# Performance work log

Hardware: AMD Instinct MI355X
Metric: run time of the kernel (lower is better)

Reference implementation:

```python
import jax, jax.numpy as jnp
import numpy as np

K = 20
EPS = 1e-5


def _bn(h, g, b, axes):
    m = jnp.mean(h, axes, keepdims=True)
    v = jnp.var(h, axes, keepdims=True)
    return (h - m) * jax.lax.rsqrt(v + EPS) * g + b


def _edge_feat(h):
    # h: [B,N,D] -> edge features [B,N,K,2D] = concat(central, neighbor-central)
    sq = jnp.sum(h * h, -1)
    # negative squared pairwise distance (larger = closer)
    adj = 2.0 * jnp.einsum('bnd,bmd->bnm', h, h) - sq[:, :, None] - sq[:, None, :]
    idx = jax.lax.top_k(adj, K)[1]  # [B,N,K] nearest (incl. self)
    nbr = jax.vmap(lambda hb, ib: hb[ib])(h, idx)  # [B,N,K,D]
    ctr = jnp.broadcast_to(h[:, :, None, :], nbr.shape)
    return jnp.concatenate([ctr, nbr - ctr], -1)


def _edge_layer(h, W, b, g, be):
    # 1x1 conv over edge features, relu THEN batchnorm (matches torch: bn(relu(conv))), max over K
    ef = _edge_feat(h)
    z = jax.nn.relu(jnp.einsum('bnkc,oc->bnko', ef, W) + b)
    z = _bn(z, g, be, (0, 1, 2))
    return jnp.max(z, axis=2)  # [B,N,O]


def _c1d(h, W, b):
    return jnp.einsum('bcl,oc->bol', h, W) + b[None, :, None]


def _bnc(h, g, b):
    m = jnp.mean(h, (0, 2), keepdims=True)
    v = jnp.var(h, (0, 2), keepdims=True)
    return (h - m) * jax.lax.rsqrt(v + EPS) * g[None, :, None] + b[None, :, None]


def _forward(x, rand_grid, W1, b1, g1, be1, W2, b2, g2, be2, W3, b3, g3, be3,
             W4, b4, g4, be4, W5, b5, g5, be5, lW, lb, lg, lbe,
             dW1, db1, dg1, dbe1, dW2, db2, dg2, dbe2, dW3, db3, dg3, dbe3, dW4, db4):
    pts = jnp.transpose(x, (0, 2, 1))  # [B,N,3]
    x1 = _edge_layer(pts, W1, b1, g1, be1)   # [B,N,64]
    x2 = _edge_layer(x1, W2, b2, g2, be2)    # [B,N,64]
    x3 = _edge_layer(x2, W3, b3, g3, be3)    # [B,N,64]
    x4 = _edge_layer(x3, W4, b4, g4, be4)    # [B,N,128]
    cat = jnp.concatenate([x1, x2, x3, x4], -1)  # [B,N,320]
    z = jax.nn.relu(jnp.einsum('bnc,oc->bno', cat, W5) + b5)
    z = _bn(z, g5, be5, (0, 1))
    glob = jnp.max(z, axis=1)  # [B,1024]
    lat = glob @ lW.T + lb
    lat = jax.nn.relu(_bn(lat, lg, lbe, (0,)))  # [B,1024]
    B, C = lat.shape
    P = rand_grid.shape[2]
    y = jnp.concatenate([rand_grid, jnp.broadcast_to(lat[:, :, None], (B, C, P))], axis=1)  # [B,1026,P]
    h = jax.nn.relu(_bnc(_c1d(y, dW1, db1), dg1, dbe1))
    h = jax.nn.relu(_bnc(_c1d(h, dW2, db2), dg2, dbe2))
    h = jax.nn.relu(_bnc(_c1d(h, dW3, db3), dg3, dbe3))
    return jnp.tanh(_c1d(h, dW4, db4))  # [B,3,P]


def setup_inputs() -> dict:
    key = jax.random.key(0)
    ks = iter(jax.random.split(key, 64))
    B, N, BOT = 8, 2048, 1024
    D = BOT + 2  # 1026
    f32 = jnp.float32

    def w(o, c):
        return jax.random.normal(next(ks), (o, c), dtype=f32) * 0.05

    def bnp(c):
        return jnp.ones((c,), f32), jnp.zeros((c,), f32)

    inp = {
        'x': jax.random.normal(next(ks), (B, 3, N), dtype=f32),
        'rand_grid': jax.random.uniform(next(ks), (B, 2, N), dtype=f32),
    }
    enc = [(64, 6), (64, 128), (64, 128), (128, 128), (1024, 320)]
    for i, (o, c) in enumerate(enc, 1):
        inp[f'W{i}'] = w(o, c)
        inp[f'b{i}'] = jnp.zeros((o,), f32)
        inp[f'g{i}'], inp[f'be{i}'] = bnp(o)
    inp['lW'] = w(BOT, 1024)
    inp['lb'] = jnp.zeros((BOT,), f32)
    inp['lg'], inp['lbe'] = bnp(BOT)
    dec = [(D, D), (D // 2, D), (D // 4, D // 2), (3, D // 4)]
    for i, (o, c) in enumerate(dec, 1):
        inp[f'dW{i}'] = w(o, c)
        inp[f'db{i}'] = jnp.zeros((o,), f32)
        if i < 4:
            inp[f'dg{i}'], inp[f'dbe{i}'] = bnp(o)
    return inp


def reference(x, rand_grid, W1, b1, g1, be1, W2, b2, g2, be2, W3, b3, g3, be3,
              W4, b4, g4, be4, W5, b5, g5, be5, lW, lb, lg, lbe,
              dW1, db1, dg1, dbe1, dW2, db2, dg2, dbe2, dW3, db3, dg3, dbe3, dW4, db4):
    return _forward(x, rand_grid, W1, b1, g1, be1, W2, b2, g2, be2, W3, b3, g3, be3,
                    W4, b4, g4, be4, W5, b5, g5, be5, lW, lb, lg, lbe,
                    dW1, db1, dg1, dbe1, dW2, db2, dg2, dbe2, dW3, db3, dg3, dbe3, dW4, db4)
```

## Files before the change

kernel.cpp:

```cpp
#include <hip/hip_runtime.h>
#include <math.h>

constexpr int NB = 8;
constexpr int NN = 2048;
constexpr int NK = 20;
constexpr int NP = 2048;


__global__ void transpose_x_kernel(const float* __restrict__ x, float* __restrict__ pts) {
  int gid = blockIdx.x * 256 + threadIdx.x;
  if (gid >= NB * NN * 3) return;
  int c = gid % 3;
  int n = (gid / 3) % NN;
  int b = gid / (3 * NN);
  pts[gid] = x[(b * 3 + c) * NN + n];
}

__global__ void transpose_mat_ld(const float* __restrict__ src, float* __restrict__ dst, int R,
                                 int C, int ldd) {
  __shared__ float tile[32][33];
  int c0 = blockIdx.x * 32, r0 = blockIdx.y * 32;
  int tx = threadIdx.x & 31, ty = threadIdx.x >> 5;
  for (int i = ty; i < 32; i += 8) {
    int r = r0 + i, c = c0 + tx;
    tile[i][tx] = (r < R && c < C) ? src[(size_t)r * C + c] : 0.f;
  }
  __syncthreads();
  for (int i = ty; i < 32; i += 8) {
    int c = c0 + i, r = r0 + tx;
    if (r < R && c < C) dst[(size_t)c * ldd + r] = tile[tx][i];
  }
}

__global__ void knn3_fused_kernel(const float* __restrict__ pts, int* __restrict__ idx) {
  __shared__ float sm[3][NN];
  int t = threadIdx.x;
  int l = t & 63, w = t >> 6;
  int gb = blockIdx.x;
  int b = gb >> 9;
  int n0 = (gb & 511) * 4;
  const float* base = pts + (size_t)b * NN * 3;
  for (int e = t; e < NN * 3; e += 256) {
    int col = e / 3, d = e - col * 3;
    sm[d][col] = base[e];
  }
  __syncthreads();
  int n = n0 + w;
  float c0 = sm[0][n], c1 = sm[1][n], c2 = sm[2][n];
  float v[32];
#pragma unroll
  for (int j = 0; j < 32; j++) {
    int col = j * 64 + l;
    float d0 = c0 - sm[0][col];
    float d1 = c1 - sm[1][col];
    float d2 = c2 - sm[2][col];
    float acc = 0.f;
    acc = fmaf(d0, d0, acc);
    acc = fmaf(d1, d1, acc);
    acc = fmaf(d2, d2, acc);
    v[j] = -acc;
  }
  int mykm = 0;
  for (int k = 0; k < NK; k++) {
    float bv = v[0];
    int bj = 0;
#pragma unroll
    for (int j = 1; j < 32; j++) {
      if (v[j] > bv) { bv = v[j]; bj = j; }
    }
    int gm = bj * 64 + l;
#pragma unroll
    for (int off = 32; off; off >>= 1) {
      float ov = __shfl_xor(bv, off, 64);
      int om = __shfl_xor(gm, off, 64);
      if (ov > bv || (ov == bv && om < gm)) { bv = ov; gm = om; }
    }
    if (l == k) mykm = gm;
    int jb = gm >> 6, lb = gm & 63;
#pragma unroll
    for (int j = 0; j < 32; j++)
      if (j == jb && l == lb) v[j] = -3e38f;
  }
  if (l < NK) idx[((size_t)(b * NN + n)) * NK + l] = mykm;
}

__global__ __launch_bounds__(256, 2) void knn64_fused4_kernel(const float* __restrict__ h, int ld,
                                                              int coff, int* __restrict__ idx) {
  __shared__ float sft[64][128];
  __shared__ float sctr[16][64];
  int t = threadIdx.x;
  int l = t & 63, w = t >> 6;
  int n0 = blockIdx.x * 16;
  int b = blockIdx.y;
  const float* rows = h + (size_t)b * NN * ld + coff;
  for (int e = t; e < 16 * 64; e += 256) {
    int r = e >> 6, d = e & 63;
    sctr[r][d] = rows[(size_t)(n0 + r) * ld + d];
  }
  int colg = t & 127;
  int dh = (t >> 7) * 32;
  float v[4][32];
#pragma unroll
  for (int ct = 0; ct < 16; ct++) {
    __syncthreads();
    {
      const float* src = &rows[(size_t)(ct * 128 + colg) * ld + dh];
#pragma unroll
      for (int q = 0; q < 8; q++) {
        float4 f = *(const float4*)(src + q * 4);
        sft[dh + q * 4 + 0][colg] = f.x;
        sft[dh + q * 4 + 1][colg] = f.y;
        sft[dh + q * 4 + 2][colg] = f.z;
        sft[dh + q * 4 + 3][colg] = f.w;
      }
    }
    __syncthreads();
    float a00 = 0.f, a01 = 0.f, a10 = 0.f, a11 = 0.f;
    float a20 = 0.f, a21 = 0.f, a30 = 0.f, a31 = 0.f;
#pragma unroll 8
    for (int d = 0; d < 64; d++) {
      float f0 = sft[d][l];
      float f1 = sft[d][64 + l];
      float c0v = sctr[4 * w + 0][d];
      float c1v = sctr[4 * w + 1][d];
      float c2v = sctr[4 * w + 2][d];
      float c3v = sctr[4 * w + 3][d];
      float e;
      e = c0v - f0; a00 = fmaf(e, e, a00);
      e = c0v - f1; a01 = fmaf(e, e, a01);
      e = c1v - f0; a10 = fmaf(e, e, a10);
      e = c1v - f1; a11 = fmaf(e, e, a11);
      e = c2v - f0; a20 = fmaf(e, e, a20);
      e = c2v - f1; a21 = fmaf(e, e, a21);
      e = c3v - f0; a30 = fmaf(e, e, a30);
      e = c3v - f1; a31 = fmaf(e, e, a31);
    }
    v[0][2 * ct] = -a00; v[0][2 * ct + 1] = -a01;
    v[1][2 * ct] = -a10; v[1][2 * ct + 1] = -a11;
    v[2][2 * ct] = -a20; v[2][2 * ct + 1] = -a21;
    v[3][2 * ct] = -a30; v[3][2 * ct + 1] = -a31;
  }
#pragma unroll
  for (int ci = 0; ci < 4; ci++) {
    int mykm = 0;
    for (int k = 0; k < NK; k++) {
      float bv = v[ci][0];
      int bj = 0;
#pragma unroll
      for (int j = 1; j < 32; j++) {
        if (v[ci][j] > bv) { bv = v[ci][j]; bj = j; }
      }
      int gm = ((bj >> 1) << 7) + ((bj & 1) << 6) + l;
#pragma unroll
      for (int off = 32; off; off >>= 1) {
        float ov = __shfl_xor(bv, off, 64);
        int om = __shfl_xor(gm, off, 64);
        if (ov > bv || (ov == bv && om < gm)) { bv = ov; gm = om; }
      }
      if (l == k) mykm = gm;
      int jb = ((gm >> 7) << 1) + ((gm >> 6) & 1);
      int lb = gm & 63;
#pragma unroll
      for (int j = 0; j < 32; j++)
        if (j == jb && l == lb) v[ci][j] = -3e38f;
    }
    if (l < NK) idx[((size_t)(b * NN + n0 + 4 * w + ci)) * NK + l] = mykm;
  }
}

__global__ void weff_kernel(const float* __restrict__ W, int O, int D, float* __restrict__ Weff) {
  int i = blockIdx.x * 256 + threadIdx.x;
  if (i >= 2 * O * D) return;
  int o = i / D, d = i - o * D;
  float v;
  if (o < O) v = W[(size_t)o * 2 * D + d] - W[(size_t)o * 2 * D + D + d];
  else v = W[(size_t)(o - O) * 2 * D + D + d];
  Weff[i] = v;
}

template <int M2, int D>
__global__ __launch_bounds__(256, 4) void pgemm_kernel(const float* __restrict__ h, int ld,
                                                       int coff, const float* __restrict__ Weff,
                                                       const float* __restrict__ bias,
                                                       float* __restrict__ P) {
  constexpr int O = M2 / 2;
  constexpr int GRP = 256 / M2;
  constexpr int NR = 8 / GRP;
  __shared__ float sh[8][D == 3 ? 4 : 68];
  int t = threadIdx.x;
  int n0 = blockIdx.x * 8;
  const float* base = h + coff;
  if constexpr (D == 64) {
    if (t < 128) {
      int r = t >> 4, q = (t & 15) * 4;
      *(float4*)&sh[r][q] = *(const float4*)&base[(size_t)(n0 + r) * ld + q];
    }
  } else {
    if (t < 24) {
      int r = t / 3, c = t - r * 3;
      sh[r][c] = base[(size_t)(n0 + r) * ld + c];
    }
  }
  __syncthreads();
  int o = t % M2;
  int gi = t / M2;
  float acc[NR];
  float bz = (o < O) ? bias[o] : 0.f;
#pragma unroll
  for (int j = 0; j < NR; j++) acc[j] = bz;
  const float* wr = Weff + (size_t)o * D;
  if constexpr (D == 64) {
#pragma unroll
    for (int d4 = 0; d4 < 16; d4++) {
      float4 w4 = *(const float4*)&wr[d4 * 4];
#pragma unroll
      for (int j = 0; j < NR; j++) {
        float4 e4 = *(const float4*)&sh[gi * NR + j][d4 * 4];
        acc[j] = fmaf(w4.x, e4.x, acc[j]);
        acc[j] = fmaf(w4.y, e4.y, acc[j]);
        acc[j] = fmaf(w4.z, e4.z, acc[j]);
        acc[j] = fmaf(w4.w, e4.w, acc[j]);
      }
    }
  } else {
    float w0 = wr[0], w1 = wr[1], w2 = wr[2];
#pragma unroll
    for (int j = 0; j < NR; j++) {
      int r = gi * NR + j;
      acc[j] = fmaf(w0, sh[r][0], fmaf(w1, sh[r][1], fmaf(w2, sh[r][2], acc[j])));
    }
  }
#pragma unroll
  for (int j = 0; j < NR; j++)
    P[(size_t)(n0 + gi * NR + j) * M2 + o] = acc[j];
}

template <int O>
__global__ __launch_bounds__(256, 8) void combine_kernel(const float* __restrict__ P,
                                                         const int* __restrict__ idx,
                                                         float* __restrict__ zmax,
                                                         float* __restrict__ zmin,
                                                         float* __restrict__ psum,
                                                         float* __restrict__ psq) {
  constexpr int CPB = 256 / O;
  constexpr int M2 = 2 * O;
  __shared__ int sidx[CPB * NK];
  int t = threadIdx.x;
  int bn0 = blockIdx.x * CPB;
  if (t < CPB * NK) sidx[t] = idx[(size_t)bn0 * NK + t];
  __syncthreads();
  int g = t / O, o = t % O;
  int bn = bn0 + g;
  int b = bn >> 11;
  float p1 = P[(size_t)bn * M2 + o];
  const float* P2 = P + (size_t)b * NN * M2 + O + o;
  float s = 0.f, sq = 0.f, mx = -3e38f, mn = 3e38f;
#pragma unroll
  for (int k = 0; k < NK; k++) {
    int nb = sidx[g * NK + k];
    float z = fmaxf(p1 + P2[(size_t)nb * M2], 0.f);
    s += z;
    sq = fmaf(z, z, sq);
    mx = fmaxf(mx, z);
    mn = fminf(mn, z);
  }
  zmax[(size_t)bn * O + o] = mx;
  zmin[(size_t)bn * O + o] = mn;
  psum[(size_t)o * (NB * NN) + bn] = s;
  psq[(size_t)o * (NB * NN) + bn] = sq;
}

__global__ void edge_reduce_kernel(const float* __restrict__ psum, const float* __restrict__ psq,
                                   const float* __restrict__ g, const float* __restrict__ be,
                                   float* __restrict__ scale, float* __restrict__ shift,
                                   double inv_n) {
  int o = blockIdx.x, t = threadIdx.x;
  double s = 0.0, q = 0.0;
  const float* ps = psum + (size_t)o * (NB * NN);
  const float* pq = psq + (size_t)o * (NB * NN);
  for (int i = t; i < NB * NN; i += 256) { s += (double)ps[i]; q += (double)pq[i]; }
  __shared__ double rs[256], rq[256];
  rs[t] = s; rq[t] = q;
  __syncthreads();
  for (int st = 128; st; st >>= 1) {
    if (t < st) { rs[t] += rs[t + st]; rq[t] += rq[t + st]; }
    __syncthreads();
  }
  if (t == 0) {
    double mean = rs[0] * inv_n;
    double var = rq[0] * inv_n - mean * mean;
    double r = 1.0 / sqrt(var + 1e-5);
    double sc = (double)g[o] * r;
    scale[o] = (float)sc;
    shift[o] = (float)((double)be[o] - mean * sc);
  }
}

__global__ void edge_affine_kernel(const float* __restrict__ zmax, const float* __restrict__ zmin,
                                   const float* __restrict__ scale, const float* __restrict__ shift,
                                   float* __restrict__ cat, int O, int coff_out) {
  int gid = blockIdx.x * 256 + threadIdx.x;
  int o = gid % O;
  int bn = gid / O;
  float sc = scale[o];
  float v = (sc >= 0.f) ? zmax[gid] : zmin[gid];
  cat[(size_t)bn * 320 + coff_out + o] = fmaf(sc, v, shift[o]);
}

__global__ __launch_bounds__(256, 2) void gemm5_64_kernel(const float* __restrict__ cat,
                                                          const float* __restrict__ W5t,
                                                          const float* __restrict__ b5,
                                                          float* __restrict__ z5) {
  __shared__ float sA[32][64];
  __shared__ float sB[32][128];
  int t = threadIdx.x;
  int r0 = blockIdx.x * 64, m0 = blockIdx.y * 128;
  int arow = t & 63, ach = (t >> 6) * 8;
  int blr = t >> 4, blc = (t & 15) * 8;
  int tx = t & 15, ty = t >> 4;
  float acc[4][8] = {};
  float rA[8], rB[16];

  auto gload = [&](int c0) {
    const float* pa = &cat[(size_t)(r0 + arow) * 320 + c0 + ach];
    float4 a0 = *(const float4*)pa;
    float4 a1 = *(const float4*)(pa + 4);
    rA[0] = a0.x; rA[1] = a0.y; rA[2] = a0.z; rA[3] = a0.w;
    rA[4] = a1.x; rA[5] = a1.y; rA[6] = a1.z; rA[7] = a1.w;
    const float* pb = &W5t[(size_t)(c0 + blr) * 1024 + m0 + blc];
    float4 b0 = *(const float4*)pb;
    float4 b1 = *(const float4*)(pb + 4);
    rB[0] = b0.x; rB[1] = b0.y; rB[2] = b0.z; rB[3] = b0.w;
    rB[4] = b1.x; rB[5] = b1.y; rB[6] = b1.z; rB[7] = b1.w;
    const float* pb2 = &W5t[(size_t)(c0 + 16 + blr) * 1024 + m0 + blc];
    float4 c4 = *(const float4*)pb2;
    float4 c5 = *(const float4*)(pb2 + 4);
    rB[8] = c4.x; rB[9] = c4.y; rB[10] = c4.z; rB[11] = c4.w;
    rB[12] = c5.x; rB[13] = c5.y; rB[14] = c5.z; rB[15] = c5.w;
  };
  auto ldswrite = [&]() {
#pragma unroll
    for (int j = 0; j < 8; j++) sA[ach + j][arow] = rA[j];
    float4 w0, w1;
    w0.x = rB[0]; w0.y = rB[1]; w0.z = rB[2]; w0.w = rB[3];
    w1.x = rB[4]; w1.y = rB[5]; w1.z = rB[6]; w1.w = rB[7];
    *(float4*)&sB[blr][blc] = w0;
    *(float4*)&sB[blr][blc + 4] = w1;
    w0.x = rB[8]; w0.y = rB[9]; w0.z = rB[10]; w0.w = rB[11];
    w1.x = rB[12]; w1.y = rB[13]; w1.z = rB[14]; w1.w = rB[15];
    *(float4*)&sB[16 + blr][blc] = w0;
    *(float4*)&sB[16 + blr][blc + 4] = w1;
  };

  gload(0);
  for (int kt = 0; kt < 10; kt++) {
    __syncthreads();
    ldswrite();
    __syncthreads();
    if (kt + 1 < 10) gload((kt + 1) * 32);
#pragma unroll
    for (int c = 0; c < 32; c++) {
      float4 a0 = *(const float4*)&sA[c][ty * 4];
      float4 b0 = *(const float4*)&sB[c][tx * 4];
      float4 b1 = *(const float4*)&sB[c][64 + tx * 4];
      float av[4] = {a0.x, a0.y, a0.z, a0.w};
      float bv[8] = {b0.x, b0.y, b0.z, b0.w, b1.x, b1.y, b1.z, b1.w};
#pragma unroll
      for (int i = 0; i < 4; i++)
#pragma unroll
        for (int j = 0; j < 8; j++) acc[i][j] = fmaf(av[i], bv[j], acc[i][j]);
    }
  }
  float bj[8];
#pragma unroll
  for (int j = 0; j < 8; j++)
    bj[j] = b5[m0 + (j < 4 ? tx * 4 + j : 64 + tx * 4 + (j - 4))];
#pragma unroll
  for (int i = 0; i < 4; i++) {
    int r = r0 + ty * 4 + i;
    float* dst = &z5[(size_t)r * 1024 + m0];
    float4 q0, q1;
    q0.x = fmaxf(acc[i][0] + bj[0], 0.f);
    q0.y = fmaxf(acc[i][1] + bj[1], 0.f);
    q0.z = fmaxf(acc[i][2] + bj[2], 0.f);
    q0.w = fmaxf(acc[i][3] + bj[3], 0.f);
    q1.x = fmaxf(acc[i][4] + bj[4], 0.f);
    q1.y = fmaxf(acc[i][5] + bj[5], 0.f);
    q1.z = fmaxf(acc[i][6] + bj[6], 0.f);
    q1.w = fmaxf(acc[i][7] + bj[7], 0.f);
    *(float4*)&dst[tx * 4] = q0;
    *(float4*)&dst[64 + tx * 4] = q1;
  }
}

__global__ void stats5_kernel(const float* __restrict__ z5, double* __restrict__ psum5,
                              double* __restrict__ psq5, float* __restrict__ pmax5,
                              float* __restrict__ pmin5) {
  int j = blockIdx.x, t = threadIdx.x;
  int row0 = j * 64;
  double s0 = 0, s1 = 0, s2 = 0, s3 = 0, q0 = 0, q1 = 0, q2 = 0, q3 = 0;
  float4 mx = {-3e38f, -3e38f, -3e38f, -3e38f}, mn = {3e38f, 3e38f, 3e38f, 3e38f};
  for (int r = 0; r < 64; r++) {
    float4 v = *(const float4*)&z5[(size_t)(row0 + r) * 1024 + t * 4];
    s0 += v.x; s1 += v.y; s2 += v.z; s3 += v.w;
    q0 += (double)v.x * v.x; q1 += (double)v.y * v.y;
    q2 += (double)v.z * v.z; q3 += (double)v.w * v.w;
    mx.x = fmaxf(mx.x, v.x); mx.y = fmaxf(mx.y, v.y); mx.z = fmaxf(mx.z, v.z); mx.w = fmaxf(mx.w, v.w);
    mn.x = fminf(mn.x, v.x); mn.y = fminf(mn.y, v.y); mn.z = fminf(mn.z, v.z); mn.w = fminf(mn.w, v.w);
  }
  size_t base = (size_t)j * 1024 + t * 4;
  psum5[base + 0] = s0; psum5[base + 1] = s1; psum5[base + 2] = s2; psum5[base + 3] = s3;
  psq5[base + 0] = q0; psq5[base + 1] = q1; psq5[base + 2] = q2; psq5[base + 3] = q3;
  *(float4*)&pmax5[base] = mx;
  *(float4*)&pmin5[base] = mn;
}

__global__ void reduce5_glob_kernel(const double* __restrict__ psum5, const double* __restrict__ psq5,
                                    const float* __restrict__ pmax5, const float* __restrict__ pmin5,
                                    const float* __restrict__ g5, const float* __restrict__ be5,
                                    float* __restrict__ glob) {
  int o = blockIdx.x * 256 + threadIdx.x;
  double s = 0.0, q = 0.0;
  for (int j = 0; j < 256; j++) {
    s += psum5[(size_t)j * 1024 + o];
    q += psq5[(size_t)j * 1024 + o];
  }
  double mean = s * (1.0 / 16384.0);
  double var = q * (1.0 / 16384.0) - mean * mean;
  double r = 1.0 / sqrt(var + 1e-5);
  double scd = (double)g5[o] * r;
  float sc = (float)scd;
  float sh = (float)((double)be5[o] - mean * scd);
  for (int b = 0; b < 8; b++) {
    float m;
    if (sc >= 0.f) {
      m = -3e38f;
      for (int jj = 0; jj < 32; jj++) m = fmaxf(m, pmax5[(size_t)(b * 32 + jj) * 1024 + o]);
    } else {
      m = 3e38f;
      for (int jj = 0; jj < 32; jj++) m = fminf(m, pmin5[(size_t)(b * 32 + jj) * 1024 + o]);
    }
    glob[b * 1024 + o] = fmaf(sc, m, sh);
  }
}

__global__ void fc_kernel(const float* __restrict__ in, const float* __restrict__ Wt, int ld,
                          int coff, const float* __restrict__ bias, float* __restrict__ out,
                          int Ci, int Co) {
  __shared__ float sin_[1024];
  __shared__ float red[8][32];
  int b = blockIdx.x, t = threadIdx.x;
  for (int e = t; e < Ci; e += 256) sin_[e] = in[(size_t)b * Ci + e];
  __syncthreads();
  int o = blockIdx.y * 32 + (t & 31);
  int cg = t >> 5;
  int cn = Ci / 8;
  float p = 0.f;
  if (o < Co) {
    for (int c = cg * cn; c < (cg + 1) * cn; c++)
      p = fmaf(Wt[(size_t)(c + coff) * ld + o], sin_[c], p);
  }
  red[cg][t & 31] = p;
  __syncthreads();
  if (cg == 0 && o < Co) {
    float s = red[0][t] + red[1][t] + red[2][t] + red[3][t] + red[4][t] + red[5][t] + red[6][t] +
              red[7][t];
    out[(size_t)b * Co + o] = s + bias[o];
  }
}

__global__ void lat_bn_kernel(const float* __restrict__ latp, const float* __restrict__ lg,
                              const float* __restrict__ lbe, float* __restrict__ lat) {
  int o = blockIdx.x * 256 + threadIdx.x;
  float v[8];
  double s = 0.0, q = 0.0;
  for (int b = 0; b < 8; b++) {
    v[b] = latp[b * 1024 + o];
    s += (double)v[b];
    q += (double)v[b] * (double)v[b];
  }
  double mean = s * 0.125;
  double var = q * 0.125 - mean * mean;
  double r = 1.0 / sqrt(var + 1e-5);
  double gd = (double)lg[o], bd = (double)lbe[o];
  for (int b = 0; b < 8; b++) {
    float z = (float)(((double)v[b] - mean) * r * gd + bd);
    lat[b * 1024 + o] = fmaxf(z, 0.f);
  }
}

__global__ void dec1_z_kernel(const float* __restrict__ rg, const float* __restrict__ dW1t,
                              const float* __restrict__ u, float* __restrict__ z1) {
  int bo = blockIdx.x;
  int b = bo / 1026;
  int o = bo - b * 1026;
  int t = threadIdx.x;
  float w0 = dW1t[o], w1 = dW1t[1026 + o], ub = u[bo];
  const float4* r0 = (const float4*)(rg + (size_t)b * 2 * NP);
  const float4* r1 = (const float4*)(rg + (size_t)b * 2 * NP + NP);
  float4* zr = (float4*)(z1 + (size_t)bo * NP);
  for (int i = t; i < NP / 4; i += 256) {
    float4 a = r0[i], c = r1[i], rr;
    rr.x = fmaf(w0, a.x, fmaf(w1, c.x, ub));
    rr.y = fmaf(w0, a.y, fmaf(w1, c.y, ub));
    rr.z = fmaf(w0, a.z, fmaf(w1, c.z, ub));
    rr.w = fmaf(w0, a.w, fmaf(w1, c.w, ub));
    zr[i] = rr;
  }
}

__global__ void dstats_kernel(const float* __restrict__ z, int C, const float* __restrict__ g,
                              const float* __restrict__ be, float* __restrict__ scale,
                              float* __restrict__ shift) {
  int o = blockIdx.x, t = threadIdx.x;
  double s = 0.0, q = 0.0;
  for (int b = 0; b < 8; b++) {
    const float4* row = (const float4*)(z + ((size_t)b * C + o) * NP);
    for (int i = t; i < NP / 4; i += 256) {
      float4 v = row[i];
      s += (double)v.x + (double)v.y + (double)v.z + (double)v.w;
      q += (double)v.x * v.x + (double)v.y * v.y + (double)v.z * v.z + (double)v.w * v.w;
    }
  }
  __shared__ double rs[256], rq[256];
  rs[t] = s; rq[t] = q;
  __syncthreads();
  for (int st = 128; st; st >>= 1) {
    if (t < st) { rs[t] += rs[t + st]; rq[t] += rq[t + st]; }
    __syncthreads();
  }
  if (t == 0) {
    double inv = 1.0 / (8.0 * NP);
    double mean = rs[0] * inv;
    double var = rq[0] * inv - mean * mean;
    double r = 1.0 / sqrt(var + 1e-5);
    double sc = (double)g[o] * r;
    scale[o] = (float)sc;
    shift[o] = (float)((double)be[o] - mean * sc);
  }
}

template <int NMT>
__global__ __launch_bounds__(256, 2) void dec_gemm64s_kernel(
    const float* __restrict__ zin, const float* __restrict__ Wt, int ldA,
    const float* __restrict__ bias, const float* __restrict__ scale,
    const float* __restrict__ shift, float* __restrict__ zout, int Ci, int Co) {
  __shared__ float sA[32][64];
  __shared__ float sB[32][128];
  int bid = blockIdx.x;
  int gl = bid & 7;
  int q = bid >> 3;
  int gh = q / NMT;
  int mt = q - gh * NMT;
  int g = gl + (gh << 3);
  int pt = g & 15;
  int b = g >> 4;
  int m0 = mt * 64, p0 = pt * 128;
  int t = threadIdx.x;
  int lr = t >> 4, lcA = (t & 15) * 4, lcB = (t & 15) * 8;
  int tx = t & 15, ty = t >> 4;
  int numK = (Ci + 31) >> 5;
  float acc[4][8] = {};
  float rA[8], rB[16];

  auto gloadhalf = [&](int c, float* ra, float* rb) {
#pragma unroll
    for (int j = 0; j < 4; j++) ra[j] = 0.f;
#pragma unroll
    for (int j = 0; j < 8; j++) rb[j] = 0.f;
    if (c < Ci) {
      int mb = m0 + lcA;
      if (mb + 4 <= Co) {
        float4 a0 = *(const float4*)&Wt[(size_t)c * ldA + mb];
        ra[0] = a0.x; ra[1] = a0.y; ra[2] = a0.z; ra[3] = a0.w;
      } else {
#pragma unroll
        for (int j = 0; j < 4; j++)
          if (mb + j < Co) ra[j] = Wt[(size_t)c * ldA + mb + j];
      }
      float sc = scale[c], sh = shift[c];
      const float* src = &zin[((size_t)b * Ci + c) * NP + p0 + lcB];
      float4 z0 = *(const float4*)src;
      float4 z1 = *(const float4*)(src + 4);
      rb[0] = fmaxf(fmaf(sc, z0.x, sh), 0.f);
      rb[1] = fmaxf(fmaf(sc, z0.y, sh), 0.f);
      rb[2] = fmaxf(fmaf(sc, z0.z, sh), 0.f);
      rb[3] = fmaxf(fmaf(sc, z0.w, sh), 0.f);
      rb[4] = fmaxf(fmaf(sc, z1.x, sh), 0.f);
      rb[5] = fmaxf(fmaf(sc, z1.y, sh), 0.f);
      rb[6] = fmaxf(fmaf(sc, z1.z, sh), 0.f);
      rb[7] = fmaxf(fmaf(sc, z1.w, sh), 0.f);
    }
  };
  auto gload = [&](int kt) {
    gloadhalf(kt * 32 + lr, rA, rB);
    gloadhalf(kt * 32 + 16 + lr, rA + 4, rB + 8);
  };
  auto ldswrite = [&]() {
    float4 v0;
    v0.x = rA[0]; v0.y = rA[1]; v0.z = rA[2]; v0.w = rA[3];
    *(float4*)&sA[lr][lcA] = v0;
    v0.x = rA[4]; v0.y = rA[5]; v0.z = rA[6]; v0.w = rA[7];
    *(float4*)&sA[16 + lr][lcA] = v0;
    float4 w0, w1;
    w0.x = rB[0]; w0.y = rB[1]; w0.z = rB[2]; w0.w = rB[3];
    w1.x = rB[4]; w1.y = rB[5]; w1.z = rB[6]; w1.w = rB[7];
    *(float4*)&sB[lr][lcB] = w0;
    *(float4*)&sB[lr][lcB + 4] = w1;
    w0.x = rB[8]; w0.y = rB[9]; w0.z = rB[10]; w0.w = rB[11];
    w1.x = rB[12]; w1.y = rB[13]; w1.z = rB[14]; w1.w = rB[15];
    *(float4*)&sB[16 + lr][lcB] = w0;
    *(float4*)&sB[16 + lr][lcB + 4] = w1;
  };

  gload(0);
  for (int kt = 0; kt < numK; kt++) {
    __syncthreads();
    ldswrite();
    __syncthreads();
    if (kt + 1 < numK) gload(kt + 1);
#pragma unroll
    for (int c = 0; c < 32; c++) {
      float4 a0 = *(const float4*)&sA[c][ty * 4];
      float4 b0 = *(const float4*)&sB[c][tx * 4];
      float4 b1 = *(const float4*)&sB[c][64 + tx * 4];
      float av[4] = {a0.x, a0.y, a0.z, a0.w};
      float bv[8] = {b0.x, b0.y, b0.z, b0.w, b1.x, b1.y, b1.z, b1.w};
#pragma unroll
      for (int i = 0; i < 4; i++)
#pragma unroll
        for (int j = 0; j < 8; j++) acc[i][j] = fmaf(av[i], bv[j], acc[i][j]);
    }
  }
#pragma unroll
  for (int i = 0; i < 4; i++) {
    int m = m0 + ty * 4 + i;
    if (m < Co) {
      float bv = bias[m];
      float* dst = &zout[((size_t)b * Co + m) * NP + p0];
      float4 q0, q1;
      q0.x = acc[i][0] + bv; q0.y = acc[i][1] + bv;
      q0.z = acc[i][2] + bv; q0.w = acc[i][3] + bv;
      q1.x = acc[i][4] + bv; q1.y = acc[i][5] + bv;
      q1.z = acc[i][6] + bv; q1.w = acc[i][7] + bv;
      *(float4*)&dst[tx * 4] = q0;
      *(float4*)&dst[64 + tx * 4] = q1;
    }
  }
}

__global__ void dec_final_kernel(const float* __restrict__ z3, const float* __restrict__ dW4,
                                 const float* __restrict__ db4, const float* __restrict__ scale,
                                 const float* __restrict__ shift, float* __restrict__ out) {
  __shared__ float w4[3 * 256];
  __shared__ float sc[256], sh[256];
  __shared__ float red[4][64][3];
  int b = blockIdx.x, pc = blockIdx.y, t = threadIdx.x;
  for (int e = t; e < 768; e += 256) w4[e] = dW4[e];
  sc[t] = scale[t];
  sh[t] = shift[t];
  __syncthreads();
  int tp = t & 63, tc = t >> 6;
  int p = pc * 64 + tp;
  float a0 = 0.f, a1 = 0.f, a2 = 0.f;
  for (int c = tc * 64; c < tc * 64 + 64; c++) {
    float hv = fmaxf(fmaf(sc[c], z3[((size_t)(b * 256 + c)) * NP + p], sh[c]), 0.f);
    a0 = fmaf(w4[c], hv, a0);
    a1 = fmaf(w4[256 + c], hv, a1);
    a2 = fmaf(w4[512 + c], hv, a2);
  }
  red[tc][tp][0] = a0;
  red[tc][tp][1] = a1;
  red[tc][tp][2] = a2;
  __syncthreads();
  if (tc == 0) {
    a0 = red[0][tp][0] + red[1][tp][0] + red[2][tp][0] + red[3][tp][0];
    a1 = red[0][tp][1] + red[1][tp][1] + red[2][tp][1] + red[3][tp][1];
    a2 = red[0][tp][2] + red[1][tp][2] + red[2][tp][2] + red[3][tp][2];
    out[((size_t)b * 3 + 0) * NP + p] = tanhf(a0 + db4[0]);
    out[((size_t)b * 3 + 1) * NP + p] = tanhf(a1 + db4[1]);
    out[((size_t)b * 3 + 2) * NP + p] = tanhf(a2 + db4[2]);
  }
}


extern "C" void kernel_launch(void* const* d_in, const int* in_sizes, int n_in, void* d_out,
                              int out_size, void* d_ws, size_t ws_size, hipStream_t stream) {
  const float* x = (const float*)d_in[0];
  const float* rg = (const float*)d_in[1];
  const float* W1 = (const float*)d_in[2];
  const float* b1 = (const float*)d_in[3];
  const float* g1 = (const float*)d_in[4];
  const float* be1 = (const float*)d_in[5];
  const float* W2 = (const float*)d_in[6];
  const float* b2 = (const float*)d_in[7];
  const float* g2 = (const float*)d_in[8];
  const float* be2 = (const float*)d_in[9];
  const float* W3 = (const float*)d_in[10];
  const float* b3 = (const float*)d_in[11];
  const float* g3 = (const float*)d_in[12];
  const float* be3 = (const float*)d_in[13];
  const float* W4 = (const float*)d_in[14];
  const float* b4 = (const float*)d_in[15];
  const float* g4 = (const float*)d_in[16];
  const float* be4 = (const float*)d_in[17];
  const float* W5 = (const float*)d_in[18];
  const float* b5 = (const float*)d_in[19];
  const float* g5 = (const float*)d_in[20];
  const float* be5 = (const float*)d_in[21];
  const float* lW = (const float*)d_in[22];
  const float* lb = (const float*)d_in[23];
  const float* lg = (const float*)d_in[24];
  const float* lbe = (const float*)d_in[25];
  const float* dW1 = (const float*)d_in[26];
  const float* db1 = (const float*)d_in[27];
  const float* dg1 = (const float*)d_in[28];
  const float* dbe1 = (const float*)d_in[29];
  const float* dW2 = (const float*)d_in[30];
  const float* db2 = (const float*)d_in[31];
  const float* dg2 = (const float*)d_in[32];
  const float* dbe2 = (const float*)d_in[33];
  const float* dW3 = (const float*)d_in[34];
  const float* db3 = (const float*)d_in[35];
  const float* dg3 = (const float*)d_in[36];
  const float* dbe3 = (const float*)d_in[37];
  const float* dW4 = (const float*)d_in[38];
  const float* db4 = (const float*)d_in[39];
  float* out = (float*)d_out;

  float* ws = (float*)d_ws;
  size_t off = 0;
  auto alloc = [&](size_t n) {
    size_t r = off;
    off += (n + 255) & ~(size_t)255;
    return r;
  };
  size_t f_pts = alloc((size_t)NB * NN * 3);
  size_t f_uA = alloc(13959168);
  size_t f_cat = f_uA;
  size_t f_idx = f_cat + 5242880;
  size_t f_zmax = f_idx + 327680;
  size_t f_zmin = f_zmax + 2097152;
  size_t f_psum = f_zmin + 2097152;
  size_t f_psq = f_psum + 2097152;
  size_t f_z2 = f_uA;
  size_t f_uB = alloc(16809984);
  size_t f_z5 = f_uB, f_z1 = f_uB;
  float* P = ws + f_uB;
  size_t f_uC = alloc(4194304);
  double* ps5_d = (double*)(ws + f_uC);
  double* pq5_d = ps5_d + 262144;
  size_t f_pM5 = f_uC + 2097152;
  size_t f_pm5 = f_pM5 + 262144;
  size_t f_z3 = f_uC;
  size_t f_weff = alloc(256 * 64);
  size_t f_W5t = alloc(320 * 1024);
  size_t f_lWt = alloc(1024 * 1024);
  size_t f_dW1t = alloc((size_t)1026 * 1026);
  size_t f_dW2t = alloc((size_t)1026 * 516);
  size_t f_dW3t = alloc(513 * 256);
  size_t f_scale = alloc(2048);
  size_t f_shift = alloc(2048);
  size_t f_glob = alloc(8 * 1024);
  size_t f_latp = alloc(8 * 1024);
  size_t f_lat = alloc(8 * 1024);
  size_t f_u = alloc(8 * 1026);
  (void)ws_size;
  (void)in_sizes;
  (void)n_in;
  (void)out_size;

  float* cat = ws + f_cat;
  int* idxp = (int*)(ws + f_idx);
  float* zmax = ws + f_zmax;
  float* zmin = ws + f_zmin;
  float* psumf = ws + f_psum;
  float* psqf = ws + f_psq;
  float* weff = ws + f_weff;
  float* scale = ws + f_scale;
  float* shift = ws + f_shift;
  const double invn_e = 1.0 / (double)(NB * NN * NK);

  transpose_x_kernel<<<192, 256, 0, stream>>>(x, ws + f_pts);
  transpose_mat_ld<<<dim3(10, 32), 256, 0, stream>>>(W5, ws + f_W5t, 1024, 320, 1024);
  transpose_mat_ld<<<dim3(32, 32), 256, 0, stream>>>(lW, ws + f_lWt, 1024, 1024, 1024);
  transpose_mat_ld<<<dim3(33, 33), 256, 0, stream>>>(dW1, ws + f_dW1t, 1026, 1026, 1026);
  transpose_mat_ld<<<dim3(33, 17), 256, 0, stream>>>(dW2, ws + f_dW2t, 513, 1026, 516);
  transpose_mat_ld<<<dim3(17, 8), 256, 0, stream>>>(dW3, ws + f_dW3t, 256, 513, 256);

  knn3_fused_kernel<<<NB * NN / 4, 256, 0, stream>>>(ws + f_pts, idxp);
  weff_kernel<<<2, 256, 0, stream>>>(W1, 64, 3, weff);
  pgemm_kernel<128, 3><<<2048, 256, 0, stream>>>(ws + f_pts, 3, 0, weff, b1, P);
  combine_kernel<64><<<4096, 256, 0, stream>>>(P, idxp, zmax, zmin, psumf, psqf);
  edge_reduce_kernel<<<64, 256, 0, stream>>>(psumf, psqf, g1, be1, scale, shift, invn_e);
  edge_affine_kernel<<<NB * NN * 64 / 256, 256, 0, stream>>>(zmax, zmin, scale, shift, cat, 64, 0);
  knn64_fused4_kernel<<<dim3(128, 8), 256, 0, stream>>>(cat, 320, 0, idxp);
  weff_kernel<<<32, 256, 0, stream>>>(W2, 64, 64, weff);
  pgemm_kernel<128, 64><<<2048, 256, 0, stream>>>(cat, 320, 0, weff, b2, P);
  combine_kernel<64><<<4096, 256, 0, stream>>>(P, idxp, zmax, zmin, psumf, psqf);
  edge_reduce_kernel<<<64, 256, 0, stream>>>(psumf, psqf, g2, be2, scale, shift, invn_e);
  edge_affine_kernel<<<NB * NN * 64 / 256, 256, 0, stream>>>(zmax, zmin, scale, shift, cat, 64, 64);
  knn64_fused4_kernel<<<dim3(128, 8), 256, 0, stream>>>(cat, 320, 64, idxp);
  weff_kernel<<<32, 256, 0, stream>>>(W3, 64, 64, weff);
  pgemm_kernel<128, 64><<<2048, 256, 0, stream>>>(cat, 320, 64, weff, b3, P);
  combine_kernel<64><<<4096, 256, 0, stream>>>(P, idxp, zmax, zmin, psumf, psqf);
  edge_reduce_kernel<<<64, 256, 0, stream>>>(psumf, psqf, g3, be3, scale, shift, invn_e);
  edge_affine_kernel<<<NB * NN * 64 / 256, 256, 0, stream>>>(zmax, zmin, scale, shift, cat, 64, 128);
  knn64_fused4_kernel<<<dim3(128, 8), 256, 0, stream>>>(cat, 320, 128, idxp);
  weff_kernel<<<64, 256, 0, stream>>>(W4, 128, 64, weff);
  pgemm_kernel<256, 64><<<2048, 256, 0, stream>>>(cat, 320, 128, weff, b4, P);
  combine_kernel<128><<<8192, 256, 0, stream>>>(P, idxp, zmax, zmin, psumf, psqf);
  edge_reduce_kernel<<<128, 256, 0, stream>>>(psumf, psqf, g4, be4, scale, shift, invn_e);
  edge_affine_kernel<<<NB * NN * 128 / 256, 256, 0, stream>>>(zmax, zmin, scale, shift, cat, 128, 192);

  gemm5_64_kernel<<<dim3(256, 8), 256, 0, stream>>>(cat, ws + f_W5t, b5, ws + f_z5);
  stats5_kernel<<<256, 256, 0, stream>>>(ws + f_z5, ps5_d, pq5_d, ws + f_pM5, ws + f_pm5);
  reduce5_glob_kernel<<<4, 256, 0, stream>>>(ps5_d, pq5_d, ws + f_pM5, ws + f_pm5, g5, be5,
                                             ws + f_glob);
  fc_kernel<<<dim3(8, 32), 256, 0, stream>>>(ws + f_glob, ws + f_lWt, 1024, 0, lb, ws + f_latp,
                                             1024, 1024);
  lat_bn_kernel<<<4, 256, 0, stream>>>(ws + f_latp, lg, lbe, ws + f_lat);
  fc_kernel<<<dim3(8, 33), 256, 0, stream>>>(ws + f_lat, ws + f_dW1t, 1026, 2, db1, ws + f_u, 1024,
                                             1026);
  dec1_z_kernel<<<8 * 1026, 256, 0, stream>>>(rg, ws + f_dW1t, ws + f_u, ws + f_z1);
  dstats_kernel<<<1026, 256, 0, stream>>>(ws + f_z1, 1026, dg1, dbe1, scale, shift);
  dec_gemm64s_kernel<9><<<9 * 128, 256, 0, stream>>>(ws + f_z1, ws + f_dW2t, 516, db2, scale,
                                                     shift, ws + f_z2, 1026, 513);
  dstats_kernel<<<513, 256, 0, stream>>>(ws + f_z2, 513, dg2, dbe2, scale, shift);
  dec_gemm64s_kernel<4><<<4 * 128, 256, 0, stream>>>(ws + f_z2, ws + f_dW3t, 256, db3, scale,
                                                     shift, ws + f_z3, 513, 256);
  dstats_kernel<<<256, 256, 0, stream>>>(ws + f_z3, 256, dg3, dbe3, scale, shift);
  dec_final_kernel<<<dim3(8, 32), 256, 0, stream>>>(ws + f_z3, dW4, db4, scale, shift, out);
}
```

Measured before the change: 2.019 ms.

## Use 1024-thread blocks with two query points per wave in 64-dim kNN

```diff
diff --git a/kernel.cpp b/kernel.cpp
--- a/kernel.cpp
+++ b/kernel.cpp
@@ -84,64 +84,58 @@
   if (l < NK) idx[((size_t)(b * NN + n)) * NK + l] = mykm;
 }
 
-__global__ __launch_bounds__(256, 2) void knn64_fused4_kernel(const float* __restrict__ h, int ld,
-                                                              int coff, int* __restrict__ idx) {
+__global__ __launch_bounds__(1024, 4) void knn64_fused2_kernel(const float* __restrict__ h,
+                                                               int ld, int coff,
+                                                               int* __restrict__ idx) {
   __shared__ float sft[64][128];
-  __shared__ float sctr[16][64];
+  __shared__ float sctr[32][64];
   int t = threadIdx.x;
   int l = t & 63, w = t >> 6;
-  int n0 = blockIdx.x * 16;
+  int n0 = blockIdx.x * 32;
   int b = blockIdx.y;
   const float* rows = h + (size_t)b * NN * ld + coff;
-  for (int e = t; e < 16 * 64; e += 256) {
+  for (int e = t; e < 32 * 64; e += 1024) {
     int r = e >> 6, d = e & 63;
     sctr[r][d] = rows[(size_t)(n0 + r) * ld + d];
   }
   int colg = t & 127;
-  int dh = (t >> 7) * 32;
-  float v[4][32];
+  int dh = (t >> 7) * 8;
+  float v[2][32];
 #pragma unroll
   for (int ct = 0; ct < 16; ct++) {
     __syncthreads();
     {
       const float* src = &rows[(size_t)(ct * 128 + colg) * ld + dh];
-#pragma unroll
-      for (int q = 0; q < 8; q++) {
-        float4 f = *(const float4*)(src + q * 4);
-        sft[dh + q * 4 + 0][colg] = f.x;
-        sft[dh + q * 4 + 1][colg] = f.y;
-        sft[dh + q * 4 + 2][colg] = f.z;
-        sft[dh + q * 4 + 3][colg] = f.w;
-      }
+      float4 f0 = *(const float4*)src;
+      float4 f1 = *(const float4*)(src + 4);
+      sft[dh + 0][colg] = f0.x;
+      sft[dh + 1][colg] = f0.y;
+      sft[dh + 2][colg] = f0.z;
+      sft[dh + 3][colg] = f0.w;
+      sft[dh + 4][colg] = f1.x;
+      sft[dh + 5][colg] = f1.y;
+      sft[dh + 6][colg] = f1.z;
+      sft[dh + 7][colg] = f1.w;
     }
     __syncthreads();
     float a00 = 0.f, a01 = 0.f, a10 = 0.f, a11 = 0.f;
-    float a20 = 0.f, a21 = 0.f, a30 = 0.f, a31 = 0.f;
 #pragma unroll 8
     for (int d = 0; d < 64; d++) {
       float f0 = sft[d][l];
       float f1 = sft[d][64 + l];
-      float c0v = sctr[4 * w + 0][d];
-      float c1v = sctr[4 * w + 1][d];
-      float c2v = sctr[4 * w + 2][d];
-      float c3v = sctr[4 * w + 3][d];
+      float c0v = sctr[2 * w + 0][d];
+      float c1v = sctr[2 * w + 1][d];
       float e;
       e = c0v - f0; a00 = fmaf(e, e, a00);
       e = c0v - f1; a01 = fmaf(e, e, a01);
       e = c1v - f0; a10 = fmaf(e, e, a10);
       e = c1v - f1; a11 = fmaf(e, e, a11);
-      e = c2v - f0; a20 = fmaf(e, e, a20);
-      e = c2v - f1; a21 = fmaf(e, e, a21);
-      e = c3v - f0; a30 = fmaf(e, e, a30);
-      e = c3v - f1; a31 = fmaf(e, e, a31);
     }
     v[0][2 * ct] = -a00; v[0][2 * ct + 1] = -a01;
     v[1][2 * ct] = -a10; v[1][2 * ct + 1] = -a11;
-    v[2][2 * ct] = -a20; v[2][2 * ct + 1] = -a21;
-    v[3][2 * ct] = -a30; v[3][2 * ct + 1] = -a31;
-  }
-#pragma unroll
-  for (int ci = 0; ci < 4; ci++) {
+  }
+#pragma unroll
+  for (int ci = 0; ci < 2; ci++) {
     int mykm = 0;
     for (int k = 0; k < NK; k++) {
       float bv = v[ci][0];
@@ -164,7 +158,7 @@
       for (int j = 0; j < 32; j++)
         if (j == jb && l == lb) v[ci][j] = -3e38f;
     }
-    if (l < NK) idx[((size_t)(b * NN + n0 + 4 * w + ci)) * NK + l] = mykm;
+    if (l < NK) idx[((size_t)(b * NN + n0 + 2 * w + ci)) * NK + l] = mykm;
   }
 }
 
@@ -794,19 +788,19 @@
   combine_kernel<64><<<4096, 256, 0, stream>>>(P, idxp, zmax, zmin, psumf, psqf);
   edge_reduce_kernel<<<64, 256, 0, stream>>>(psumf, psqf, g1, be1, scale, shift, invn_e);
   edge_affine_kernel<<<NB * NN * 64 / 256, 256, 0, stream>>>(zmax, zmin, scale, shift, cat, 64, 0);
-  knn64_fused4_kernel<<<dim3(128, 8), 256, 0, stream>>>(cat, 320, 0, idxp);
+  knn64_fused2_kernel<<<dim3(64, 8), 1024, 0, stream>>>(cat, 320, 0, idxp);
   weff_kernel<<<32, 256, 0, stream>>>(W2, 64, 64, weff);
   pgemm_kernel<128, 64><<<2048, 256, 0, stream>>>(cat, 320, 0, weff, b2, P);
   combine_kernel<64><<<4096, 256, 0, stream>>>(P, idxp, zmax, zmin, psumf, psqf);
   edge_reduce_kernel<<<64, 256, 0, stream>>>(psumf, psqf, g2, be2, scale, shift, invn_e);
   edge_affine_kernel<<<NB * NN * 64 / 256, 256, 0, stream>>>(zmax, zmin, scale, shift, cat, 64, 64);
-  knn64_fused4_kernel<<<dim3(128, 8), 256, 0, stream>>>(cat, 320, 64, idxp);
+  knn64_fused2_kernel<<<dim3(64, 8), 1024, 0, stream>>>(cat, 320, 64, idxp);
   weff_kernel<<<32, 256, 0, stream>>>(W3, 64, 64, weff);
   pgemm_kernel<128, 64><<<2048, 256, 0, stream>>>(cat, 320, 64, weff, b3, P);
   combine_kernel<64><<<4096, 256, 0, stream>>>(P, idxp, zmax, zmin, psumf, psqf);
   edge_reduce_kernel<<<64, 256, 0, stream>>>(psumf, psqf, g3, be3, scale, shift, invn_e);
   edge_affine_kernel<<<NB * NN * 64 / 256, 256, 0, stream>>>(zmax, zmin, scale, shift, cat, 64, 128);
-  knn64_fused4_kernel<<<dim3(128, 8), 256, 0, stream>>>(cat, 320, 128, idxp);
+  knn64_fused2_kernel<<<dim3(64, 8), 1024, 0, stream>>>(cat, 320, 128, idxp);
   weff_kernel<<<64, 256, 0, stream>>>(W4, 128, 64, weff);
   pgemm_kernel<256, 64><<<2048, 256, 0, stream>>>(cat, 320, 128, weff, b4, P);
   combine_kernel<128><<<8192, 256, 0, stream>>>(P, idxp, zmax, zmin, psumf, psqf);
```

After: 1.831 ms. 9.3% less time.
